# Kernel optimization log

Measured on AMD Instinct MI355X. Metric: run time of the kernel, lower is better.

The kernel has to match this reference:

```python
import jax, jax.numpy as jnp
import numpy as np

B, T, I, H, L, O = 256, 336, 16, 512, 256, 10


def setup_inputs() -> dict:
    key = jax.random.key(0)
    ks = jax.random.split(key, 24)
    n = lambda k, s, sc=1.0: jax.random.normal(k, s, dtype=jnp.float32) * sc
    mask = lambda k, s: (jax.random.uniform(k, s) > 0.5).astype(jnp.float32) * 2.0  # dropout p=0.5
    return {
        "x": n(ks[0], (B, T, I)),
        # dropout masks (inverted-dropout scaling already applied)
        "drop_x": mask(ks[1], (B, T, I)),
        "drop_h": mask(ks[2], (B, H)),
        "drop_l": mask(ks[3], (B, L)),
        # BayesianLSTM variational params + reparameterization noise
        "wih_mu": n(ks[4], (I, 4 * H), 0.05), "wih_rho": jnp.full((I, 4 * H), -5.0, jnp.float32), "eps_wih": n(ks[5], (I, 4 * H)),
        "whh_mu": n(ks[6], (H, 4 * H), 0.05), "whh_rho": jnp.full((H, 4 * H), -5.0, jnp.float32), "eps_whh": n(ks[7], (H, 4 * H)),
        "b_mu": n(ks[8], (4 * H,), 0.05), "b_rho": jnp.full((4 * H,), -5.0, jnp.float32), "eps_b": n(ks[9], (4 * H,)),
        # BayesianLinear variational params + noise (weight is [out, in])
        "blw_mu": n(ks[10], (L, H), 0.05), "blw_rho": jnp.full((L, H), -5.0, jnp.float32), "eps_blw": n(ks[11], (L, H)),
        "blb_mu": n(ks[12], (L,), 0.05), "blb_rho": jnp.full((L,), -5.0, jnp.float32), "eps_blb": n(ks[13], (L,)),
        # final deterministic linear, no bias
        "lin_w": n(ks[14], (O, L), 0.05),
    }


def _forward(x, drop_x, drop_h, drop_l,
             wih_mu, wih_rho, eps_wih, whh_mu, whh_rho, eps_whh,
             b_mu, b_rho, eps_b, blw_mu, blw_rho, eps_blw,
             blb_mu, blb_rho, eps_blb, lin_w):
    sp = jax.nn.softplus
    # sample weights: w = mu + softplus(rho) * eps
    Wih = wih_mu + sp(wih_rho) * eps_wih        # [I, 4H]
    Whh = whh_mu + sp(whh_rho) * eps_whh        # [H, 4H]
    b = b_mu + sp(b_rho) * eps_b                # [4H]
    BLW = blw_mu + sp(blw_rho) * eps_blw        # [L, H]
    BLb = blb_mu + sp(blb_rho) * eps_blb        # [L]

    xd = x * drop_x                             # dropout on input
    # precompute input-to-gate projection for all timesteps: [B, T, 4H]
    xg = jnp.einsum('bti,ig->btg', xd, Wih) + b

    def step(carry, xg_t):
        h, c = carry
        gates = xg_t + h @ Whh                  # [B, 4H]
        i, f, g, o = jnp.split(gates, 4, axis=-1)
        i = jax.nn.sigmoid(i)
        f = jax.nn.sigmoid(f)
        g = jnp.tanh(g)
        o = jax.nn.sigmoid(o)
        c = f * c + i * g
        h = o * jnp.tanh(c)
        return (h, c), h

    h0 = jnp.zeros((x.shape[0], Whh.shape[0]), x.dtype)
    (_, _), hs = jax.lax.scan(step, (h0, h0), jnp.swapaxes(xg, 0, 1))  # hs: [T, B, H]
    hidden_seq = jnp.swapaxes(hs, 0, 1)         # blitz returns batch-major [B, T, H]
    # faithful to lstm_out.view(sequence_length, len(x), hidden_dim)[-1] (reshape, not transpose)
    last = hidden_seq.reshape(T, x.shape[0], -1)[-1]    # [B, H]

    y = jax.nn.relu((last * drop_h) @ BLW.T + BLb)      # Bayesian linear + ReLU
    return (y * drop_l) @ lin_w.T                       # final linear, no bias


def reference(x, drop_x, drop_h, drop_l,
              wih_mu, wih_rho, eps_wih, whh_mu, whh_rho, eps_whh,
              b_mu, b_rho, eps_b, blw_mu, blw_rho, eps_blw,
              blb_mu, blb_rho, eps_blb, lin_w):
    return _forward(x, drop_x, drop_h, drop_l,
                    wih_mu, wih_rho, eps_wih, whh_mu, whh_rho, eps_whh,
                    b_mu, b_rho, eps_b, blw_mu, blw_rho, eps_blw,
                    blb_mu, blb_rho, eps_blb, lin_w)
```

## Files before the change

kernel.cpp:

```cpp
#include <hip/hip_runtime.h>

#define T_STEPS 336
#define NWG 32
#define NREP 4

typedef unsigned long long u64;

__device__ float g_h[337 * 512];
__device__ float g_blw[256 * 512];
__device__ u64   g_rep[NREP][2][8][64];

__device__ __forceinline__ float softplus_f(float x) {
  return (x > 20.f) ? x : log1pf(__expf(x));
}
__device__ __forceinline__ float sigmoid_f(float x) {
  return 1.f / (1.f + __expf(-x));
}
__device__ __forceinline__ float tanh_f(float x) {
  x = fminf(fmaxf(x, -15.f), 15.f);
  float e = __expf(-2.f * x);
  return (1.f - e) / (1.f + e);
}

__global__ __launch_bounds__(512) void lstm_kernel(
    const float* __restrict__ x, const float* __restrict__ drop_x,
    const float* __restrict__ wih_mu, const float* __restrict__ wih_rho, const float* __restrict__ eps_wih,
    const float* __restrict__ b_mu, const float* __restrict__ b_rho, const float* __restrict__ eps_b,
    const float* __restrict__ whh_mu, const float* __restrict__ whh_rho, const float* __restrict__ eps_whh,
    const float* __restrict__ blw_mu, const float* __restrict__ blw_rho, const float* __restrict__ eps_blw)
{
  const int r = blockIdx.x;
  const int tid = threadIdx.x;
  const int cl = tid & 63;
  const int seg = tid >> 6;
  const int gate = cl >> 4, kl = cl & 15;
  const int col = gate * 512 + r * 16 + kl;
  const int row0 = seg * 64;
  const int rep = r & (NREP - 1);

  if (tid < 16) {
    const int idx = r * 16 + tid;
    const int sw = idx >> 6, sc = idx & 63;
    #pragma unroll
    for (int q = 0; q < NREP; ++q) {
      __hip_atomic_store(&g_rep[q][0][sw][sc], 0ULL, __ATOMIC_RELAXED, __HIP_MEMORY_SCOPE_AGENT);
      __hip_atomic_store(&g_rep[q][1][sw][sc], 0ULL, __ATOMIC_RELAXED, __HIP_MEMORY_SCOPE_AGENT);
    }
  }

  __shared__ float xd[336 * 16];
  __shared__ float hs[512];
  __shared__ float part[2][8][64];

  {
    const int e0 = (r * 512 + tid) * 8;
    #pragma unroll
    for (int q = 0; q < 8; ++q) {
      const int e = e0 + q;
      g_blw[e] = blw_mu[e] + softplus_f(blw_rho[e]) * eps_blw[e];
    }
  }

  for (int e = tid; e < 5376; e += 512) {
    const int src = 255 * 5376 + e;
    xd[e] = x[src] * drop_x[src];
  }

  float w[64];
  #pragma unroll
  for (int j = 0; j < 64; ++j) {
    const int idx = (row0 + j) * 2048 + col;
    w[j] = whh_mu[idx] + softplus_f(whh_rho[idx]) * eps_whh[idx];
  }

  float wih[16];
  float bias = 0.f;
  if (tid < 64) {
    bias = b_mu[col] + softplus_f(b_rho[col]) * eps_b[col];
    #pragma unroll
    for (int i = 0; i < 16; ++i) {
      const int idx = i * 2048 + col;
      wih[i] = wih_mu[idx] + softplus_f(wih_rho[idx]) * eps_wih[idx];
    }
  }
  __syncthreads();

  auto xg_at = [&](int t) -> float {
    const float4* xr = (const float4*)(xd + t * 16);
    float4 x0 = xr[0], x1 = xr[1], x2 = xr[2], x3 = xr[3];
    float s0 = fmaf(x0.x, wih[0], bias);
    s0 = fmaf(x0.y, wih[1], s0); s0 = fmaf(x0.z, wih[2], s0); s0 = fmaf(x0.w, wih[3], s0);
    float s1 = x1.x * wih[4];
    s1 = fmaf(x1.y, wih[5], s1); s1 = fmaf(x1.z, wih[6], s1); s1 = fmaf(x1.w, wih[7], s1);
    float s2 = x2.x * wih[8];
    s2 = fmaf(x2.y, wih[9], s2); s2 = fmaf(x2.z, wih[10], s2); s2 = fmaf(x2.w, wih[11], s2);
    float s3 = x3.x * wih[12];
    s3 = fmaf(x3.y, wih[13], s3); s3 = fmaf(x3.z, wih[14], s3); s3 = fmaf(x3.w, wih[15], s3);
    return (s0 + s1) + (s2 + s3);
  };

  float c = 0.f;
  float xgv = (tid < 64) ? xg_at(0) : 0.f;

  for (int t = 0; t < T_STEPS; ++t) {
    const int p = t & 1;

    {
      const u64* slot = &g_rep[rep][p][seg][cl];
      u64 v;
      int it = 0;
      for (;;) {
        v = __hip_atomic_load(slot, __ATOMIC_RELAXED, __HIP_MEMORY_SCOPE_AGENT);
        if ((unsigned)(v >> 32) == (unsigned)t) break;
        if (++it > (1 << 22)) break;
      }
      hs[tid] = __uint_as_float((unsigned)v);
    }

    float a0 = 0.f, a1 = 0.f, a2 = 0.f, a3 = 0.f;
    const float4* hv = (const float4*)(hs + row0);
    #pragma unroll
    for (int jj = 0; jj < 16; ++jj) {
      float4 h4 = hv[jj];
      a0 = fmaf(h4.x, w[4 * jj],     a0);
      a1 = fmaf(h4.y, w[4 * jj + 1], a1);
      a2 = fmaf(h4.z, w[4 * jj + 2], a2);
      a3 = fmaf(h4.w, w[4 * jj + 3], a3);
    }
    part[p][seg][cl] = (a0 + a1) + (a2 + a3);
    __syncthreads();

    if (tid < 64) {
      float g = xgv
              + ((part[p][0][tid] + part[p][1][tid]) + (part[p][2][tid] + part[p][3][tid]))
              + ((part[p][4][tid] + part[p][5][tid]) + (part[p][6][tid] + part[p][7][tid]));
      const bool is_g = (gate == 2);
      float xin = is_g ? 2.f * fminf(fmaxf(g, -15.f), 15.f) : g;
      float s = sigmoid_f(xin);
      float act = is_g ? 2.f * s - 1.f : s;
      float vi = __shfl(act, kl);
      float vf = __shfl(act, kl + 16);
      float vg = __shfl(act, kl + 32);
      float vo = __shfl(act, kl + 48);
      if (tid < 16) {
        c = vf * c + vi * vg;
        float h = vo * tanh_f(c);
        const int idx = r * 16 + tid;
        const int sw = idx >> 6, sc = idx & 63;
        u64 pv = (((u64)(unsigned)(t + 1)) << 32) | (u64)__float_as_uint(h);
        #pragma unroll
        for (int q = 0; q < NREP; ++q)
          __hip_atomic_store(&g_rep[q][(t + 1) & 1][sw][sc], pv,
                             __ATOMIC_RELAXED, __HIP_MEMORY_SCOPE_AGENT);
        g_h[(t + 1) * 512 + idx] = h;
      }
      if (t + 1 < T_STEPS) xgv = xg_at(t + 1);
    }
  }
}

__global__ __launch_bounds__(256) void head_kernel(
    const float* __restrict__ drop_h, const float* __restrict__ drop_l,
    const float* __restrict__ blb_mu, const float* __restrict__ blb_rho,
    const float* __restrict__ eps_blb,
    const float* __restrict__ lin_w, float* __restrict__ out)
{
  const int j = blockIdx.x, tid = threadIdx.x;
  __shared__ float hd[512];
  __shared__ float y[256];

  for (int k = tid; k < 512; k += 256)
    hd[k] = g_h[(81 + j) * 512 + k] * drop_h[j * 512 + k];
  __syncthreads();

  {
    const int l = tid;
    float acc = blb_mu[l] + softplus_f(blb_rho[l]) * eps_blb[l];
    const float* wrow = g_blw + l * 512;
    #pragma unroll 8
    for (int k = 0; k < 512; ++k) acc = fmaf(hd[k], wrow[k], acc);
    acc = fmaxf(acc, 0.f);
    y[l] = acc * drop_l[j * 256 + l];
  }
  __syncthreads();

  if (tid < 10) {
    float acc = 0.f;
    const float* lrow = lin_w + tid * 256;
    #pragma unroll 8
    for (int l = 0; l < 256; ++l) acc = fmaf(y[l], lrow[l], acc);
    out[j * 10 + tid] = acc;
  }
}

extern "C" void kernel_launch(void* const* d_in, const int* in_sizes, int n_in,
                              void* d_out, int out_size, void* d_ws, size_t ws_size,
                              hipStream_t stream) {
  const float* x        = (const float*)d_in[0];
  const float* drop_x   = (const float*)d_in[1];
  const float* drop_h   = (const float*)d_in[2];
  const float* drop_l   = (const float*)d_in[3];
  const float* wih_mu   = (const float*)d_in[4];
  const float* wih_rho  = (const float*)d_in[5];
  const float* eps_wih  = (const float*)d_in[6];
  const float* whh_mu   = (const float*)d_in[7];
  const float* whh_rho  = (const float*)d_in[8];
  const float* eps_whh  = (const float*)d_in[9];
  const float* b_mu     = (const float*)d_in[10];
  const float* b_rho    = (const float*)d_in[11];
  const float* eps_b    = (const float*)d_in[12];
  const float* blw_mu   = (const float*)d_in[13];
  const float* blw_rho  = (const float*)d_in[14];
  const float* eps_blw  = (const float*)d_in[15];
  const float* blb_mu   = (const float*)d_in[16];
  const float* blb_rho  = (const float*)d_in[17];
  const float* eps_blb  = (const float*)d_in[18];
  const float* lin_w    = (const float*)d_in[19];

  lstm_kernel<<<NWG, 512, 0, stream>>>(x, drop_x,
                                       wih_mu, wih_rho, eps_wih,
                                       b_mu, b_rho, eps_b,
                                       whh_mu, whh_rho, eps_whh,
                                       blw_mu, blw_rho, eps_blw);

  head_kernel<<<256, 256, 0, stream>>>(drop_h, drop_l,
                                       blb_mu, blb_rho, eps_blb,
                                       lin_w, (float*)d_out);
}
```

Measured before the change: 687.1 us.

## Fuse Bayesian linear head into the LSTM kernel and capture hidden states in LDS

Drops the separate head kernel and the global g_h/g_blw buffers. Each of the 32 workgroups keeps the 8 hidden-state rows it needs in shared memory while they are broadcast during the recurrence. After the loop it samples the BLW weights on the fly and computes the linear+ReLU+final linear for those 8 outputs. This removes a kernel launch, global stores from the recurrent critical path, and a round trip through global memory. In exchange, every workgroup re-samples the full BLW matrix, which means redundant softplus work and memory traffic. The last workgroup also has to wait for the final timestep.

```diff
diff --git a/kernel.cpp b/kernel.cpp
--- a/kernel.cpp
+++ b/kernel.cpp
@@ -6,9 +6,7 @@
 
 typedef unsigned long long u64;
 
-__device__ float g_h[337 * 512];
-__device__ float g_blw[256 * 512];
-__device__ u64   g_rep[NREP][2][8][64];
+__device__ u64 g_rep[NREP][2][8][64];
 
 __device__ __forceinline__ float softplus_f(float x) {
   return (x > 20.f) ? x : log1pf(__expf(x));
@@ -27,7 +25,10 @@
     const float* __restrict__ wih_mu, const float* __restrict__ wih_rho, const float* __restrict__ eps_wih,
     const float* __restrict__ b_mu, const float* __restrict__ b_rho, const float* __restrict__ eps_b,
     const float* __restrict__ whh_mu, const float* __restrict__ whh_rho, const float* __restrict__ eps_whh,
-    const float* __restrict__ blw_mu, const float* __restrict__ blw_rho, const float* __restrict__ eps_blw)
+    const float* __restrict__ blw_mu, const float* __restrict__ blw_rho, const float* __restrict__ eps_blw,
+    const float* __restrict__ drop_h, const float* __restrict__ drop_l,
+    const float* __restrict__ blb_mu, const float* __restrict__ blb_rho, const float* __restrict__ eps_blb,
+    const float* __restrict__ lin_w, float* __restrict__ out)
 {
   const int r = blockIdx.x;
   const int tid = threadIdx.x;
@@ -51,15 +52,8 @@
   __shared__ float xd[336 * 16];
   __shared__ float hs[512];
   __shared__ float part[2][8][64];
-
-  {
-    const int e0 = (r * 512 + tid) * 8;
-    #pragma unroll
-    for (int q = 0; q < 8; ++q) {
-      const int e = e0 + q;
-      g_blw[e] = blw_mu[e] + softplus_f(blw_rho[e]) * eps_blw[e];
-    }
-  }
+  __shared__ float head_h[8][512];
+  __shared__ float party[2][8][256];
 
   for (int e = tid; e < 5376; e += 512) {
     const int src = 255 * 5376 + e;
@@ -115,6 +109,8 @@
         if (++it > (1 << 22)) break;
       }
       hs[tid] = __uint_as_float((unsigned)v);
+      if (t >= 81 && ((t - 81) >> 3) == r)
+        head_h[(t - 81) & 7][tid] = __uint_as_float((unsigned)v);
     }
 
     float a0 = 0.f, a1 = 0.f, a2 = 0.f, a3 = 0.f;
@@ -152,44 +148,69 @@
         for (int q = 0; q < NREP; ++q)
           __hip_atomic_store(&g_rep[q][(t + 1) & 1][sw][sc], pv,
                              __ATOMIC_RELAXED, __HIP_MEMORY_SCOPE_AGENT);
-        g_h[(t + 1) * 512 + idx] = h;
       }
       if (t + 1 < T_STEPS) xgv = xg_at(t + 1);
     }
   }
-}
-
-__global__ __launch_bounds__(256) void head_kernel(
-    const float* __restrict__ drop_h, const float* __restrict__ drop_l,
-    const float* __restrict__ blb_mu, const float* __restrict__ blb_rho,
-    const float* __restrict__ eps_blb,
-    const float* __restrict__ lin_w, float* __restrict__ out)
-{
-  const int j = blockIdx.x, tid = threadIdx.x;
-  __shared__ float hd[512];
-  __shared__ float y[256];
-
-  for (int k = tid; k < 512; k += 256)
-    hd[k] = g_h[(81 + j) * 512 + k] * drop_h[j * 512 + k];
+
+  if (r == 31) {
+    const u64* slot = &g_rep[rep][0][seg][cl];
+    u64 v;
+    int it = 0;
+    for (;;) {
+      v = __hip_atomic_load(slot, __ATOMIC_RELAXED, __HIP_MEMORY_SCOPE_AGENT);
+      if ((unsigned)(v >> 32) == 336u) break;
+      if (++it > (1 << 22)) break;
+    }
+    head_h[7][tid] = __uint_as_float((unsigned)v);
+  }
+
+  #pragma unroll
+  for (int jj = 0; jj < 8; ++jj)
+    head_h[jj][tid] *= drop_h[(r * 8 + jj) * 512 + tid];
   __syncthreads();
 
   {
+    const int l = tid & 255;
+    const int kh = tid >> 8;
+    const int kbase = kh * 256;
+    float acc[8] = {0.f, 0.f, 0.f, 0.f, 0.f, 0.f, 0.f, 0.f};
+    const float* mu  = blw_mu  + l * 512 + kbase;
+    const float* rho = blw_rho + l * 512 + kbase;
+    const float* ep  = eps_blw + l * 512 + kbase;
+    #pragma unroll 8
+    for (int kk = 0; kk < 256; ++kk) {
+      const float wv = mu[kk] + softplus_f(rho[kk]) * ep[kk];
+      const int k = kbase + kk;
+      #pragma unroll
+      for (int jj = 0; jj < 8; ++jj)
+        acc[jj] = fmaf(head_h[jj][k], wv, acc[jj]);
+    }
+    #pragma unroll
+    for (int jj = 0; jj < 8; ++jj) party[kh][jj][l] = acc[jj];
+  }
+  __syncthreads();
+
+  if (tid < 256) {
     const int l = tid;
-    float acc = blb_mu[l] + softplus_f(blb_rho[l]) * eps_blb[l];
-    const float* wrow = g_blw + l * 512;
+    const float b = blb_mu[l] + softplus_f(blb_rho[l]) * eps_blb[l];
+    #pragma unroll
+    for (int jj = 0; jj < 8; ++jj) {
+      const int j = r * 8 + jj;
+      float yv = fmaxf(party[0][jj][l] + party[1][jj][l] + b, 0.f);
+      party[0][jj][l] = yv * drop_l[j * 256 + l];
+    }
+  }
+  __syncthreads();
+
+  if (tid < 80) {
+    const int jj = tid / 10, o = tid - jj * 10;
+    const float* lrow = lin_w + o * 256;
+    const float* yrow = party[0][jj];
+    float acc = 0.f;
     #pragma unroll 8
-    for (int k = 0; k < 512; ++k) acc = fmaf(hd[k], wrow[k], acc);
-    acc = fmaxf(acc, 0.f);
-    y[l] = acc * drop_l[j * 256 + l];
-  }
-  __syncthreads();
-
-  if (tid < 10) {
-    float acc = 0.f;
-    const float* lrow = lin_w + tid * 256;
-    #pragma unroll 8
-    for (int l = 0; l < 256; ++l) acc = fmaf(y[l], lrow[l], acc);
-    out[j * 10 + tid] = acc;
+    for (int l2 = 0; l2 < 256; ++l2) acc = fmaf(yrow[l2], lrow[l2], acc);
+    out[(r * 8 + jj) * 10 + o] = acc;
   }
 }
 
@@ -221,9 +242,8 @@
                                        wih_mu, wih_rho, eps_wih,
                                        b_mu, b_rho, eps_b,
                                        whh_mu, whh_rho, eps_whh,
-                                       blw_mu, blw_rho, eps_blw);
-
-  head_kernel<<<256, 256, 0, stream>>>(drop_h, drop_l,
+                                       blw_mu, blw_rho, eps_blw,
+                                       drop_h, drop_l,
                                        blb_mu, blb_rho, eps_blb,
                                        lin_w, (float*)d_out);
 }
```

Result: slower. 860.9 us (+25.3%).
